# Performance work log

Measured on AMD Instinct MI355X. Metric: run time of the kernel, lower is better.

The kernel has to match this reference:

```python
import jax, jax.numpy as jnp
import numpy as np

B, T, C, H = 8, 4096, 384, 64

def setup_inputs() -> dict:
    key = jax.random.key(0)
    k1, k2, k3, k4 = jax.random.split(key, 4)
    x = jax.random.normal(k1, (B, T, C), dtype=jnp.float32)
    Wq = jax.random.normal(k2, (C, H), dtype=jnp.float32) / np.sqrt(C)
    Wk = jax.random.normal(k3, (C, H), dtype=jnp.float32) / np.sqrt(C)
    Wv = jax.random.normal(k4, (C, H), dtype=jnp.float32) / np.sqrt(C)
    return {"x": x, "Wq": Wq, "Wk": Wk, "Wv": Wv}

def reference(x, Wq, Wk, Wv):
    # single-head causal self-attention (dropout in eval mode = identity)
    T_ = x.shape[1]
    q = jnp.einsum('btc,ch->bth', x, Wq)   # [B,T,H]
    k = jnp.einsum('btc,ch->bth', x, Wk)   # [B,T,H]
    v = jnp.einsum('btc,ch->bth', x, Wv)   # [B,T,H]
    scale = 1.0 / jnp.sqrt(jnp.float32(Wq.shape[1]))
    wei = jnp.einsum('bth,bsh->bts', q, k) * scale        # [B,T,T]
    causal = jnp.tril(jnp.ones((T_, T_), dtype=bool))
    wei = jnp.where(causal, wei, -jnp.inf)
    wei = jax.nn.softmax(wei, axis=-1)
    out = jnp.einsum('bts,bsh->bth', wei, v)              # [B,T,H]
    return out
```

## Files before the change

kernel.cpp:

```cpp
#include <hip/hip_runtime.h>
#include <hip/hip_bf16.h>
#include <cstdint>
#include <cstddef>

#define BATCH 8
#define SEQ   4096
#define CDIM  384
#define HDIM  64
#define NSPL  8

typedef __attribute__((ext_vector_type(8)))  __bf16 bf16x8;
typedef __attribute__((ext_vector_type(4)))  float  f32x4;
typedef __attribute__((ext_vector_type(16))) float  f32x16;
typedef __attribute__((ext_vector_type(4)))  short  short4v;

#if __has_builtin(__builtin_amdgcn_permlane32_swap)
#define HAVE_PERMLANE 1
#else
#define HAVE_PERMLANE 0
#endif

typedef __attribute__((address_space(3))) char lds_char;
typedef const __attribute__((address_space(1))) char gbl_char;

static __device__ __forceinline__ void gl_lds16(const void* g, void* l) {
  __builtin_amdgcn_global_load_lds((gbl_char*)g, (lds_char*)l, 16, 0, 0);
}

static __device__ __forceinline__ short f2bf(float f) {
  union { float f; uint32_t u; } v; v.f = f;
  uint32_t r = v.u + 0x7fffu + ((v.u >> 16) & 1u);
  return (short)(r >> 16);
}

static __device__ __forceinline__ float bf2f(short s) {
  union { uint32_t u; float f; } t;
  t.u = ((uint32_t)(uint16_t)s) << 16;
  return t.f;
}

static __device__ __forceinline__ uint32_t cvtpk(float lo, float hi) {
  uint32_t r;
  asm("v_cvt_pk_bf16_f32 %0, %1, %2" : "=v"(r) : "v"(lo), "v"(hi));
  return r;
}

static __device__ __forceinline__ f32x4 mfma16(bf16x8 a, bf16x8 b, f32x4 c) {
  return __builtin_amdgcn_mfma_f32_16x16x32_bf16(a, b, c, 0, 0, 0);
}

static __device__ __forceinline__ f32x16 mfma32(bf16x8 a, bf16x8 b, f32x16 c) {
  return __builtin_amdgcn_mfma_f32_32x32x16_bf16(a, b, c, 0, 0, 0);
}

static __device__ __forceinline__ f32x4 zero4() {
  f32x4 z = {0.f, 0.f, 0.f, 0.f};
  return z;
}

static __device__ __forceinline__ float xhalf(float x, int hi) {
#if HAVE_PERMLANE
  union { float f; uint32_t u; } a; a.f = x;
  auto r = __builtin_amdgcn_permlane32_swap(a.u, a.u, false, false);
  union { uint32_t u; float f; } o; o.u = hi ? r[0] : r[1];
  return o.f;
#else
  return __shfl_xor(x, 32, 64);
#endif
}

static __device__ __forceinline__ void swap32(uint32_t& a, uint32_t& b, int hi) {
#if HAVE_PERMLANE
  auto r = __builtin_amdgcn_permlane32_swap(a, b, false, false);
  a = r[0]; b = r[1];
#else
  uint32_t sa = (uint32_t)__shfl_xor((int)a, 32, 64);
  uint32_t sb = (uint32_t)__shfl_xor((int)b, 32, 64);
  uint32_t na = hi ? sb : a;
  uint32_t nb = hi ? b : sa;
  a = na; b = nb;
#endif
}

static __device__ __forceinline__ float tmax16(const f32x16& v) {
  float a = fmaxf(fmaxf(v[0], v[1]), fmaxf(v[2], v[3]));
  float b = fmaxf(fmaxf(v[4], v[5]), fmaxf(v[6], v[7]));
  float c = fmaxf(fmaxf(v[8], v[9]), fmaxf(v[10], v[11]));
  float d = fmaxf(fmaxf(v[12], v[13]), fmaxf(v[14], v[15]));
  return fmaxf(fmaxf(a, b), fmaxf(c, d));
}

__global__ __launch_bounds__(256) void wpack_kernel(
    const float* __restrict__ Wq, const float* __restrict__ Wk,
    const float* __restrict__ Wv, short* __restrict__ Wt) {
  int idx = blockIdx.x * 256 + threadIdx.x;
  if (idx >= 192 * CDIM) return;
  int n = idx / CDIM;
  int c = idx - n * CDIM;
  int m = n >> 6, h = n & 63;
  const float* W = (m == 0) ? Wq : (m == 1) ? Wk : Wv;
  float s = (m == 0) ? 0.18033688011112042f : 1.0f;
  Wt[idx] = f2bf(W[c * HDIM + h] * s);
}

#define KPAD 136

__global__ __launch_bounds__(256) void qkv_kernel(
    const float* __restrict__ x, const short* __restrict__ Wt,
    short* __restrict__ qb, short* __restrict__ kb, short* __restrict__ vT) {
  __shared__ short xs[2][64][KPAD];
  const int tid = threadIdx.x;
  const int tokbase = blockIdx.x * 64;
  const float4* xg = (const float4*)(x + (size_t)tokbase * CDIM);

  for (int i = tid; i < 2048; i += 256) {
    int r = i >> 5, c4 = i & 31;
    float4 v = xg[r * 96 + c4];
    uint2 st; st.x = cvtpk(v.x, v.y); st.y = cvtpk(v.z, v.w);
    *(uint2*)&xs[0][r][c4 * 4] = st;
  }
  __syncthreads();

  const int wave = tid >> 6;
  const int lane = tid & 63;
  const int l16  = lane & 15;
  const int lq   = lane >> 4;

  f32x4 acc[4][3];
  #pragma unroll
  for (int ai = 0; ai < 4; ++ai)
    #pragma unroll
    for (int j = 0; j < 3; ++j) acc[ai][j] = zero4();

  for (int ch = 0; ch < 3; ++ch) {
    if (ch < 2) {
      const int nb = (ch + 1) & 1;
      for (int i = tid; i < 2048; i += 256) {
        int r = i >> 5, c4 = i & 31;
        float4 v = xg[r * 96 + (ch + 1) * 32 + c4];
        uint2 st; st.x = cvtpk(v.x, v.y); st.y = cvtpk(v.z, v.w);
        *(uint2*)&xs[nb][r][c4 * 4] = st;
      }
    }
    const int cb = ch & 1;
    #pragma unroll
    for (int kk = 0; kk < 4; ++kk) {
      const int k0 = kk * 32;
      bf16x8 a[4];
      #pragma unroll
      for (int ai = 0; ai < 4; ++ai)
        a[ai] = *(const bf16x8*)&xs[cb][ai * 16 + l16][k0 + lq * 8];
      bf16x8 bb[3];
      #pragma unroll
      for (int j = 0; j < 3; ++j) {
        const int nt = wave * 3 + j;
        bb[j] = *(const bf16x8*)&Wt[(size_t)(nt * 16 + l16) * CDIM +
                                    ch * 128 + k0 + lq * 8];
      }
      #pragma unroll
      for (int ai = 0; ai < 4; ++ai)
        #pragma unroll
        for (int j = 0; j < 3; ++j)
          acc[ai][j] = mfma16(a[ai], bb[j], acc[ai][j]);
    }
    __syncthreads();
  }

  const int b     = tokbase >> 12;
  const int tloc0 = tokbase & (SEQ - 1);
  #pragma unroll
  for (int j = 0; j < 3; ++j) {
    const int col = (wave * 3 + j) * 16 + l16;
    const int mat = col >> 6;
    const int h   = col & 63;
    #pragma unroll
    for (int ai = 0; ai < 4; ++ai) {
      const int row0 = ai * 16 + lq * 4;
      if (mat < 2) {
        short* dst = mat ? kb : qb;
        #pragma unroll
        for (int r = 0; r < 4; ++r)
          dst[(size_t)(tokbase + row0 + r) * HDIM + h] = f2bf(acc[ai][j][r]);
      } else {
        union { uint32_t u[2]; short4v s; } sv;
        sv.u[0] = cvtpk(acc[ai][j][0], acc[ai][j][1]);
        sv.u[1] = cvtpk(acc[ai][j][2], acc[ai][j][3]);
        *(short4v*)&vT[(size_t)(b * HDIM + h) * SEQ + (tloc0 + row0)] = sv.s;
      }
    }
  }
}

__global__ __launch_bounds__(256, 3) void attn_kernel(
    const short* __restrict__ qb, const short* __restrict__ kb,
    const short* __restrict__ vT, short* __restrict__ opart,
    float2* __restrict__ mlw) {
  __shared__ short kvbuf[2][2][4096];

  const int tid  = threadIdx.x;
  const int wave = tid >> 6;
  const int lane = tid & 63;
  const int l31  = lane & 31;
  const int hi   = lane >> 5;
  const int bid  = blockIdx.x;
  const int b    = bid & 7;
  const int idx  = bid >> 3;
  const int qt   = 31 - (idx >> 3);
  const int part = idx & 7;
  const int nkv  = 2 * qt + 2;
  const int base = nkv >> 3;
  const int rem  = nkv & 7;
  const int scnt = base + (part < rem ? 1 : 0);
  const int sbeg = part * base + (part < rem ? part : rem);
  const bool dia = (scnt > 0) && (sbeg + scnt == nkv);
  const int q0   = qt << 7;
  const int qw0  = q0 + wave * 32;
  const size_t bT = (size_t)b * SEQ;

  const char* kg = (const char*)(kb + bT * HDIM);
  const char* vg = (const char*)(vT + (size_t)b * HDIM * SEQ);

  const int rsub = lane >> 3;
  const int gcol = ((lane & 7) << 4) ^ (rsub << 4);
  const int krb  = wave * 16;

  f32x16 oacc[2];
  #pragma unroll
  for (int hb = 0; hb < 2; ++hb)
    #pragma unroll
    for (int r = 0; r < 16; ++r) oacc[hb][r] = 0.f;
  float m = -1e30f, l = 0.f;

  if (scnt > 0) {
    bf16x8 qf[4];
    {
      const short* qrow = qb + (bT + qw0 + l31) * HDIM + hi * 8;
      #pragma unroll
      for (int t = 0; t < 4; ++t)
        qf[t] = *(const bf16x8*)(qrow + 16 * t);
    }
    const int sw = (l31 & 7) << 4;
    int colk[4];
    #pragma unroll
    for (int t = 0; t < 4; ++t) colk[t] = ((t * 32) + hi * 16) ^ sw;
    const int rbase = l31 * 128;

    {
      const int sf = sbeg << 6;
      #pragma unroll
      for (int i = 0; i < 2; ++i) {
        const int r = krb + i * 8;
        gl_lds16(kg + (size_t)(sf + r + rsub) * 128 + gcol,
                 (char*)&kvbuf[0][0][0] + r * 128);
        gl_lds16(vg + (size_t)(r + rsub) * 8192 + (size_t)sf * 2 + gcol,
                 (char*)&kvbuf[0][1][0] + r * 128);
      }
    }
    __syncthreads();

    int cur = 0;
    for (int it = 0; it < scnt; ++it) {
      const int s0 = (sbeg + it) << 6;
      if (it + 1 < scnt) {
        const int s1 = s0 + 64;
        const int nb = cur ^ 1;
        #pragma unroll
        for (int i = 0; i < 2; ++i) {
          const int r = krb + i * 8;
          gl_lds16(kg + (size_t)(s1 + r + rsub) * 128 + gcol,
                   (char*)&kvbuf[nb][0][0] + r * 128);
          gl_lds16(vg + (size_t)(r + rsub) * 8192 + (size_t)s1 * 2 + gcol,
                   (char*)&kvbuf[nb][1][0] + r * 128);
        }
      }

      if (s0 <= qw0 + 31) {
        const char* bufc = (const char*)kvbuf + cur * 16384;

        f32x16 sacc[2];
        #pragma unroll
        for (int sb = 0; sb < 2; ++sb) {
          #pragma unroll
          for (int r = 0; r < 16; ++r) sacc[sb][r] = 0.f;
          #pragma unroll
          for (int t = 0; t < 4; ++t) {
            bf16x8 kf = *(const bf16x8*)(bufc + sb * 4096 + rbase + colk[t]);
            sacc[sb] = mfma32(kf, qf[t], sacc[sb]);
          }
        }

        if (s0 + 63 > qw0) {
          const int qg = qw0 + l31;
          #pragma unroll
          for (int sb = 0; sb < 2; ++sb)
            #pragma unroll
            for (int r = 0; r < 16; ++r) {
              const int sg = s0 + sb * 32 + (r & 3) + 8 * (r >> 2) + 4 * hi;
              if (sg > qg) sacc[sb][r] = -3e38f;
            }
        }

        float pm = fmaxf(tmax16(sacc[0]), tmax16(sacc[1]));
        pm = fmaxf(pm, xhalf(pm, hi));

        if (!__all(pm <= m + 8.f)) {
          const float mn = fmaxf(m, pm);
          const float sc = exp2f(m - mn);
          m = mn; l *= sc;
          #pragma unroll
          for (int hb = 0; hb < 2; ++hb)
            #pragma unroll
            for (int r = 0; r < 16; ++r) oacc[hb][r] *= sc;
        }

        float p[2][16];
        #pragma unroll
        for (int sb = 0; sb < 2; ++sb)
          #pragma unroll
          for (int r = 0; r < 16; ++r)
            p[sb][r] = exp2f(sacc[sb][r] - m);
        float t8[8];
        #pragma unroll
        for (int sb = 0; sb < 2; ++sb)
          #pragma unroll
          for (int g = 0; g < 4; ++g)
            t8[sb * 4 + g] = (p[sb][4 * g] + p[sb][4 * g + 1]) +
                             (p[sb][4 * g + 2] + p[sb][4 * g + 3]);
        float rs = ((t8[0] + t8[1]) + (t8[2] + t8[3])) +
                   ((t8[4] + t8[5]) + (t8[6] + t8[7]));
        rs += xhalf(rs, hi);
        l += rs;

        uint32_t w[2][4][2];
        #pragma unroll
        for (int sb = 0; sb < 2; ++sb)
          #pragma unroll
          for (int g = 0; g < 4; ++g) {
            w[sb][g][0] = cvtpk(p[sb][4 * g + 0], p[sb][4 * g + 1]);
            w[sb][g][1] = cvtpk(p[sb][4 * g + 2], p[sb][4 * g + 3]);
          }

        bf16x8 pf[4];
        #pragma unroll
        for (int sb = 0; sb < 2; ++sb)
          #pragma unroll
          for (int t = 0; t < 2; ++t) {
            uint32_t a0 = w[sb][2 * t][0], b0 = w[sb][2 * t + 1][0];
            uint32_t a1 = w[sb][2 * t][1], b1 = w[sb][2 * t + 1][1];
            swap32(a0, b0, hi);
            swap32(a1, b1, hi);
            union { uint32_t u[4]; bf16x8 v; } uu;
            uu.u[0] = a0; uu.u[1] = a1; uu.u[2] = b0; uu.u[3] = b1;
            pf[sb * 2 + t] = uu.v;
          }

        __builtin_amdgcn_s_setprio(1);
        #pragma unroll
        for (int hb = 0; hb < 2; ++hb)
          #pragma unroll
          for (int ks = 0; ks < 4; ++ks) {
            bf16x8 vf = *(const bf16x8*)(bufc + 8192 + hb * 4096 + rbase + colk[ks]);
            oacc[hb] = mfma32(vf, pf[ks], oacc[hb]);
          }
        __builtin_amdgcn_s_setprio(0);
      }

      __syncthreads();
      cur ^= 1;
    }
  }

  short* obase = opart + (size_t)part * ((size_t)BATCH * SEQ * HDIM);
  const int q = qw0 + l31;
  #pragma unroll
  for (int hb = 0; hb < 2; ++hb)
    #pragma unroll
    for (int g = 0; g < 4; ++g) {
      uint2 st;
      st.x = cvtpk(oacc[hb][4 * g + 0], oacc[hb][4 * g + 1]);
      st.y = cvtpk(oacc[hb][4 * g + 2], oacc[hb][4 * g + 3]);
      *(uint2*)&obase[(bT + q) * HDIM + hb * 32 + 8 * g + 4 * hi] = st;
    }
  if (lane < 32) {
    float2 ml; ml.x = m; ml.y = l;
    mlw[part * (BATCH * SEQ) + bT + q] = ml;
  }
}

__global__ __launch_bounds__(256) void merge_kernel(
    float* __restrict__ out, const short* __restrict__ opart,
    const float2* __restrict__ mlw) {
  const int g   = blockIdx.x * 256 + threadIdx.x;
  const int row = g >> 4;
  const int c4  = (g & 15) << 2;
  float2 ml[NSPL];
  float mm = -3.4e38f;
  #pragma unroll
  for (int i = 0; i < NSPL; ++i) {
    ml[i] = mlw[i * (BATCH * SEQ) + row];
    mm = fmaxf(mm, ml[i].x);
  }
  float w[NSPL];
  float ls = 0.f;
  #pragma unroll
  for (int i = 0; i < NSPL; ++i) {
    w[i] = exp2f(ml[i].x - mm);
    ls += w[i] * ml[i].y;
  }
  const size_t stride = (size_t)BATCH * SEQ * HDIM;
  const size_t off = (size_t)row * HDIM + c4;
  float a0 = 0.f, a1 = 0.f, a2 = 0.f, a3 = 0.f;
  #pragma unroll
  for (int i = 0; i < NSPL; ++i) {
    short4v s = *(const short4v*)&opart[i * stride + off];
    a0 += w[i] * bf2f(s[0]);
    a1 += w[i] * bf2f(s[1]);
    a2 += w[i] * bf2f(s[2]);
    a3 += w[i] * bf2f(s[3]);
  }
  const float inv = 1.0f / ls;
  float4 r;
  r.x = a0 * inv; r.y = a1 * inv; r.z = a2 * inv; r.w = a3 * inv;
  *(float4*)&out[off] = r;
}

extern "C" void kernel_launch(void* const* d_in, const int* in_sizes, int n_in,
                              void* d_out, int out_size, void* d_ws, size_t ws_size,
                              hipStream_t stream) {
  (void)in_sizes; (void)n_in; (void)out_size; (void)ws_size;
  const float* x  = (const float*)d_in[0];
  const float* Wq = (const float*)d_in[1];
  const float* Wk = (const float*)d_in[2];
  const float* Wv = (const float*)d_in[3];

  const size_t qkvb = (size_t)BATCH * SEQ * HDIM * sizeof(short);
  const size_t opb  = (size_t)NSPL * BATCH * SEQ * HDIM * sizeof(short);
  const size_t mlb  = (size_t)NSPL * BATCH * SEQ * sizeof(float2);
  char* ws = (char*)d_ws;
  short*  qb    = (short*)(ws);
  short*  kb    = (short*)(ws + qkvb);
  short*  vT    = (short*)(ws + 2 * qkvb);
  short*  opart = (short*)(ws + 3 * qkvb);
  float2* mlw   = (float2*)(ws + 3 * qkvb + opb);
  short*  Wt    = (short*)(ws + 3 * qkvb + opb + mlb);

  wpack_kernel<<<dim3((192 * CDIM + 255) / 256), dim3(256), 0, stream>>>(Wq, Wk, Wv, Wt);
  qkv_kernel<<<dim3(BATCH * SEQ / 64), dim3(256), 0, stream>>>(x, Wt, qb, kb, vT);
  attn_kernel<<<dim3(2048), dim3(256), 0, stream>>>(qb, kb, vT, opart, mlw);
  merge_kernel<<<dim3(BATCH * SEQ * HDIM / 4 / 256), dim3(256), 0, stream>>>(
      (float*)d_out, opart, mlw);
}
```

Measured before the change: 74.27 us.

## Single-buffer KV tiles in LDS, raise occupancy hint, use raw v_exp_f32

Drops the double-buffered K/V LDS staging in favor of one buffer that is refilled after a barrier at the end of each iteration, halving shared memory per block. The launch-bounds minimum blocks per CU rises from 3 to 8 so more waves can stay resident and hide load latency. exp2f is replaced by inline v_exp_f32, which skips the denormal and range handling, and the max reduction tree is reshaped into 3-input fmax chains. The cost is that loads are no longer overlapped with compute inside a block, and the tighter register budget may cause spills.

```diff
diff --git a/kernel.cpp b/kernel.cpp
--- a/kernel.cpp
+++ b/kernel.cpp
@@ -42,6 +42,12 @@
 static __device__ __forceinline__ uint32_t cvtpk(float lo, float hi) {
   uint32_t r;
   asm("v_cvt_pk_bf16_f32 %0, %1, %2" : "=v"(r) : "v"(lo), "v"(hi));
+  return r;
+}
+
+static __device__ __forceinline__ float fexp2(float x) {
+  float r;
+  asm("v_exp_f32 %0, %1" : "=v"(r) : "v"(x));
   return r;
 }
 
@@ -83,11 +89,14 @@
 }
 
 static __device__ __forceinline__ float tmax16(const f32x16& v) {
-  float a = fmaxf(fmaxf(v[0], v[1]), fmaxf(v[2], v[3]));
-  float b = fmaxf(fmaxf(v[4], v[5]), fmaxf(v[6], v[7]));
-  float c = fmaxf(fmaxf(v[8], v[9]), fmaxf(v[10], v[11]));
-  float d = fmaxf(fmaxf(v[12], v[13]), fmaxf(v[14], v[15]));
-  return fmaxf(fmaxf(a, b), fmaxf(c, d));
+  float a = fmaxf(fmaxf(v[0], v[1]), v[2]);
+  float b = fmaxf(fmaxf(v[3], v[4]), v[5]);
+  float c = fmaxf(fmaxf(v[6], v[7]), v[8]);
+  float d = fmaxf(fmaxf(v[9], v[10]), v[11]);
+  float e = fmaxf(fmaxf(v[12], v[13]), v[14]);
+  float f = fmaxf(fmaxf(a, b), c);
+  float g = fmaxf(fmaxf(d, e), v[15]);
+  return fmaxf(f, g);
 }
 
 __global__ __launch_bounds__(256) void wpack_kernel(
@@ -191,11 +200,11 @@
   }
 }
 
-__global__ __launch_bounds__(256, 3) void attn_kernel(
+__global__ __launch_bounds__(256, 8) void attn_kernel(
     const short* __restrict__ qb, const short* __restrict__ kb,
     const short* __restrict__ vT, short* __restrict__ opart,
     float2* __restrict__ mlw) {
-  __shared__ short kvbuf[2][2][4096];
+  __shared__ short kvbuf[2][4096];
 
   const int tid  = threadIdx.x;
   const int wave = tid >> 6;
@@ -212,7 +221,6 @@
   const int rem  = nkv & 7;
   const int scnt = base + (part < rem ? 1 : 0);
   const int sbeg = part * base + (part < rem ? part : rem);
-  const bool dia = (scnt > 0) && (sbeg + scnt == nkv);
   const int q0   = qt << 7;
   const int qw0  = q0 + wave * 32;
   const size_t bT = (size_t)b * SEQ;
@@ -251,31 +259,18 @@
       for (int i = 0; i < 2; ++i) {
         const int r = krb + i * 8;
         gl_lds16(kg + (size_t)(sf + r + rsub) * 128 + gcol,
-                 (char*)&kvbuf[0][0][0] + r * 128);
+                 (char*)&kvbuf[0][0] + r * 128);
         gl_lds16(vg + (size_t)(r + rsub) * 8192 + (size_t)sf * 2 + gcol,
-                 (char*)&kvbuf[0][1][0] + r * 128);
+                 (char*)&kvbuf[1][0] + r * 128);
       }
     }
     __syncthreads();
 
-    int cur = 0;
     for (int it = 0; it < scnt; ++it) {
       const int s0 = (sbeg + it) << 6;
-      if (it + 1 < scnt) {
-        const int s1 = s0 + 64;
-        const int nb = cur ^ 1;
-        #pragma unroll
-        for (int i = 0; i < 2; ++i) {
-          const int r = krb + i * 8;
-          gl_lds16(kg + (size_t)(s1 + r + rsub) * 128 + gcol,
-                   (char*)&kvbuf[nb][0][0] + r * 128);
-          gl_lds16(vg + (size_t)(r + rsub) * 8192 + (size_t)s1 * 2 + gcol,
-                   (char*)&kvbuf[nb][1][0] + r * 128);
-        }
-      }
 
       if (s0 <= qw0 + 31) {
-        const char* bufc = (const char*)kvbuf + cur * 16384;
+        const char* bufc = (const char*)kvbuf;
 
         f32x16 sacc[2];
         #pragma unroll
@@ -305,7 +300,7 @@
 
         if (!__all(pm <= m + 8.f)) {
           const float mn = fmaxf(m, pm);
-          const float sc = exp2f(m - mn);
+          const float sc = fexp2(m - mn);
           m = mn; l *= sc;
           #pragma unroll
           for (int hb = 0; hb < 2; ++hb)
@@ -318,7 +313,7 @@
         for (int sb = 0; sb < 2; ++sb)
           #pragma unroll
           for (int r = 0; r < 16; ++r)
-            p[sb][r] = exp2f(sacc[sb][r] - m);
+            p[sb][r] = fexp2(sacc[sb][r] - m);
         float t8[8];
         #pragma unroll
         for (int sb = 0; sb < 2; ++sb)
@@ -365,8 +360,19 @@
         __builtin_amdgcn_s_setprio(0);
       }
 
-      __syncthreads();
-      cur ^= 1;
+      if (it + 1 < scnt) {
+        __syncthreads();
+        const int s1 = s0 + 64;
+        #pragma unroll
+        for (int i = 0; i < 2; ++i) {
+          const int r = krb + i * 8;
+          gl_lds16(kg + (size_t)(s1 + r + rsub) * 128 + gcol,
+                   (char*)&kvbuf[0][0] + r * 128);
+          gl_lds16(vg + (size_t)(r + rsub) * 8192 + (size_t)s1 * 2 + gcol,
+                   (char*)&kvbuf[1][0] + r * 128);
+        }
+        __syncthreads();
+      }
     }
   }
 
@@ -404,7 +410,7 @@
   float ls = 0.f;
   #pragma unroll
   for (int i = 0; i < NSPL; ++i) {
-    w[i] = exp2f(ml[i].x - mm);
+    w[i] = fexp2(ml[i].x - mm);
     ls += w[i] * ml[i].y;
   }
   const size_t stride = (size_t)BATCH * SEQ * HDIM;
```

After: 263.0 us. 3.54x slower.
